# Optimization experiments

Measured on AMD Instinct MI355X. Metric: run time of the kernel, lower is better.

## Reference

```python
import jax, jax.numpy as jnp
import numpy as np

DIM = 768
HEADS = 12
HIDDEN = 3072  # int(dim * mlp_ratio)
DEGREE = 3
EPS = 1e-5


def layer_norm(x, g, b):
    m = jnp.mean(x, axis=-1, keepdims=True)
    v = jnp.mean((x - m) ** 2, axis=-1, keepdims=True)
    return (x - m) * jax.lax.rsqrt(v + EPS) * g + b


def cheby_layer(x, coeffs):
    # x: (B, N, I); coeffs: (I, O, DEGREE+1)
    t = jnp.tanh(x)
    theta = jnp.arccos(t)  # (B, N, I)
    d = jnp.arange(DEGREE + 1, dtype=x.dtype)
    basis = jnp.cos(theta[..., None] * d)  # (B, N, I, D)
    return jnp.einsum('bnid,iod->bno', basis, coeffs)


def setup_inputs() -> dict:
    key = jax.random.key(0)
    ks = jax.random.split(key, 9)
    B, N, C, H = 32, 197, DIM, HIDDEN
    x = jax.random.normal(ks[0], (B, N, C), dtype=jnp.float32)
    g1 = jnp.ones((C,), jnp.float32)
    b1 = jnp.zeros((C,), jnp.float32)
    w_qkv = jax.random.normal(ks[1], (C, 3 * C), jnp.float32) * (C ** -0.5)
    w_proj = jax.random.normal(ks[2], (C, C), jnp.float32) * (C ** -0.5)
    b_proj = jnp.zeros((C,), jnp.float32)
    g2 = jnp.ones((C,), jnp.float32)
    b2 = jnp.zeros((C,), jnp.float32)
    c1 = jax.random.normal(ks[3], (C, H, DEGREE + 1), jnp.float32) / (C * (DEGREE + 1))
    c2 = jax.random.normal(ks[4], (H, C, DEGREE + 1), jnp.float32) / (H * (DEGREE + 1))
    return {"x": x, "g1": g1, "b1": b1, "w_qkv": w_qkv, "w_proj": w_proj,
            "b_proj": b_proj, "g2": g2, "b2": b2, "c1": c1, "c2": c2}


def reference(x, g1, b1, w_qkv, w_proj, b_proj, g2, b2, c1, c2):
    B, N, C = x.shape
    hd = C // HEADS
    scale = hd ** -0.5
    # --- attention branch ---
    h = layer_norm(x, g1, b1)
    qkv = (h @ w_qkv).reshape(B, N, 3, HEADS, hd).transpose(2, 0, 3, 1, 4)
    q, k, v = qkv[0], qkv[1], qkv[2]  # (B, H, N, hd)
    attn = jax.nn.softmax(jnp.einsum('bhnd,bhmd->bhnm', q, k) * scale, axis=-1)
    o = jnp.einsum('bhnm,bhmd->bhnd', attn, v).transpose(0, 2, 1, 3).reshape(B, N, C)
    x = x + o @ w_proj + b_proj
    # --- ChebyKAN MLP branch ---
    h = layer_norm(x, g2, b2)
    h = cheby_layer(h, c1)   # (B, N, HIDDEN)
    h = cheby_layer(h, c2)   # (B, N, C)
    return x + h
```

## Files before the change

kernel.cpp:

```cpp
#include <hip/hip_runtime.h>
#include <hip/hip_bf16.h>
#include <cmath>
#include <cstdint>
#include <cstddef>

#define DEV __device__ __forceinline__

typedef __attribute__((ext_vector_type(4))) float f32x4;
typedef __attribute__((ext_vector_type(8))) short bf16x8;
typedef __attribute__((ext_vector_type(4))) unsigned int u32x4;
typedef __attribute__((ext_vector_type(4))) unsigned short u16x4;

constexpr int NBATCH = 32;
constexpr int SEQ    = 197;
constexpr int CH     = 768;
constexpr int H3     = 3 * CH;
constexpr int NHEADS = 12;
constexpr int HD     = 64;
constexpr int HID    = 3072;
constexpr int TOK    = NBATCH * SEQ;
constexpr int TOKP   = 6400;
constexpr int KSPLIT = 4;
constexpr float LNEPS = 1e-5f;

DEV unsigned short f2bf(float f) {
  unsigned int u = __builtin_bit_cast(unsigned int, f);
  u += 0x7fffu + ((u >> 16) & 1u);
  return (unsigned short)(u >> 16);
}
DEV float bf2f(unsigned short s) {
  unsigned int u = ((unsigned int)s) << 16;
  return __builtin_bit_cast(float, u);
}

DEV void async_copy16(void* lds, const void* gmem) {
  __builtin_amdgcn_global_load_lds(
      (const __attribute__((address_space(1))) unsigned int*)gmem,
      (__attribute__((address_space(3))) unsigned int*)lds, 16, 0, 0);
}

template <int DO_TANH>
__global__ void ln_kernel(const float* __restrict__ xin, const float* __restrict__ gg,
                          const float* __restrict__ bb, unsigned short* __restrict__ outp) {
  const int row  = blockIdx.x * 4 + (threadIdx.x >> 6);
  const int lane = threadIdx.x & 63;
  if (row >= TOK) {
    u16x4 z = {0, 0, 0, 0};
    #pragma unroll
    for (int c = 0; c < 3; ++c)
      *(u16x4*)&outp[(size_t)row * CH + c * 256 + lane * 4] = z;
    return;
  }
  f32x4 v[3];
  float s = 0.f, s2 = 0.f;
  #pragma unroll
  for (int c = 0; c < 3; ++c) {
    v[c] = *(const f32x4*)&xin[(size_t)row * CH + c * 256 + lane * 4];
    #pragma unroll
    for (int e = 0; e < 4; ++e) { s += v[c][e]; s2 += v[c][e] * v[c][e]; }
  }
  #pragma unroll
  for (int off = 32; off; off >>= 1) { s += __shfl_xor(s, off); s2 += __shfl_xor(s2, off); }
  const float mean = s * (1.f / CH);
  const float var  = s2 * (1.f / CH) - mean * mean;
  const float rs   = rsqrtf(var + LNEPS);
  #pragma unroll
  for (int c = 0; c < 3; ++c) {
    f32x4 gv = *(const f32x4*)&gg[c * 256 + lane * 4];
    f32x4 bv = *(const f32x4*)&bb[c * 256 + lane * 4];
    u16x4 o;
    #pragma unroll
    for (int e = 0; e < 4; ++e) {
      float f = (v[c][e] - mean) * rs * gv[e] + bv[e];
      if (DO_TANH) f = tanhf(f);
      o[e] = f2bf(f);
    }
    *(u16x4*)&outp[(size_t)row * CH + c * 256 + lane * 4] = o;
  }
}

__global__ void transpose_bf16(const float* __restrict__ in, unsigned short* __restrict__ outp,
                               int K, int N) {
  __shared__ unsigned short tile[64][65];
  const int k0 = blockIdx.x * 64, n0 = blockIdx.y * 64;
  const int tc = threadIdx.x & 63, tr = threadIdx.x >> 6;
  #pragma unroll
  for (int rr = 0; rr < 64; rr += 4)
    tile[rr + tr][tc] = f2bf(in[(size_t)(k0 + rr + tr) * N + n0 + tc]);
  __syncthreads();
  #pragma unroll
  for (int rr = 0; rr < 64; rr += 4)
    outp[(size_t)(n0 + rr + tr) * K + k0 + tc] = tile[tc][rr + tr];
}

__global__ void cheb_combine(const float* __restrict__ cc, unsigned short* __restrict__ outp,
                             float* __restrict__ partial, int I, int O) {
  __shared__ unsigned short t1[64][65];
  __shared__ unsigned short t2[64][65];
  __shared__ unsigned short t3[64][65];
  __shared__ float psum[4][64];
  const int i0 = blockIdx.x * 64, o0 = blockIdx.y * 64;
  const int tc = threadIdx.x & 63, tr = threadIdx.x >> 6;
  float bs = 0.f;
  #pragma unroll
  for (int rr = 0; rr < 64; rr += 4) {
    f32x4 v = *(const f32x4*)&cc[((size_t)(i0 + rr + tr) * O + (o0 + tc)) * 4];
    t1[rr + tr][tc] = f2bf(v[1] - 3.f * v[3]);
    t2[rr + tr][tc] = f2bf(2.f * v[2]);
    t3[rr + tr][tc] = f2bf(4.f * v[3]);
    bs += v[0] - v[2];
  }
  psum[tr][tc] = bs;
  __syncthreads();
  const size_t K3 = (size_t)3 * I;
  #pragma unroll
  for (int rr = 0; rr < 64; rr += 4) {
    size_t ob = (size_t)(o0 + rr + tr) * K3 + i0 + tc;
    outp[ob]         = t1[tc][rr + tr];
    outp[ob + I]     = t2[tc][rr + tr];
    outp[ob + 2 * I] = t3[tc][rr + tr];
  }
  if (tr == 0)
    partial[(size_t)blockIdx.x * O + o0 + tc] =
        psum[0][tc] + psum[1][tc] + psum[2][tc] + psum[3][tc];
}

__global__ void bias_finish(const float* __restrict__ partial, float* __restrict__ bias,
                            int nblk, int O) {
  const int o = blockIdx.x * 256 + threadIdx.x;
  float s = 0.f;
  for (int k = 0; k < nblk; ++k) s += partial[(size_t)k * O + o];
  bias[o] = s;
}

__global__ void zero_pad_rows(unsigned short* __restrict__ p) {
  const size_t idx = ((size_t)blockIdx.x * 256 + threadIdx.x) * 4;
  u16x4 z = {0, 0, 0, 0};
  *(u16x4*)&p[(size_t)TOK * CH + idx] = z;
}

template <int EPI>
__global__ __launch_bounds__(256)
void gemm_kernel(const unsigned short* __restrict__ A,
                 const unsigned short* __restrict__ BT,
                 const int K, const int Nn,
                 const float* __restrict__ bias,
                 const float* __restrict__ resid,
                 void* __restrict__ Cout) {
  __shared__ __align__(16) unsigned short As[2][128 * 32];
  __shared__ __align__(16) unsigned short Bs[2][128 * 32];
  const int t = threadIdx.x;
  const int lane = t & 63;
  const int wid = t >> 6;
  const int wm = wid >> 1, wn = wid & 1;
  const int bm = blockIdx.x * 128;
  const int bn = blockIdx.y * 128;
  const int srow = t >> 2;
  const int scol = (t & 3) * 8;
  f32x4 acc[4][4] = {};
  const int nkt = K >> 5;

  auto stage = [&](int buf, int kt) {
    const int kk = kt << 5;
    char* lb = (char*)&Bs[buf][0] + (wid << 10);
    async_copy16(lb,        &BT[(size_t)(bn + srow) * K + kk + scol]);
    async_copy16(lb + 4096, &BT[(size_t)(bn + 64 + srow) * K + kk + scol]);
    char* la = (char*)&As[buf][0] + (wid << 10);
    async_copy16(la,        &A[(size_t)(bm + srow) * K + kk + scol]);
    async_copy16(la + 4096, &A[(size_t)(bm + 64 + srow) * K + kk + scol]);
  };

  int cur = 0;
  stage(0, 0);
  for (int kt = 0; kt < nkt; ++kt) {
    if (kt + 1 < nkt) {
      stage(cur ^ 1, kt + 1);
      asm volatile("s_waitcnt vmcnt(4)" ::: "memory");
    } else {
      asm volatile("s_waitcnt vmcnt(0)" ::: "memory");
    }
    __builtin_amdgcn_s_barrier();
    __builtin_amdgcn_sched_barrier(0);
    bf16x8 af[4], bfr[4];
    const int frow = lane & 15;
    const int fk = (lane >> 4) * 8;
    #pragma unroll
    for (int m = 0; m < 4; ++m)
      af[m] = *(const bf16x8*)&As[cur][(wm * 64 + m * 16 + frow) * 32 + fk];
    #pragma unroll
    for (int n = 0; n < 4; ++n)
      bfr[n] = *(const bf16x8*)&Bs[cur][(wn * 64 + n * 16 + frow) * 32 + fk];
    #pragma unroll
    for (int m = 0; m < 4; ++m)
      #pragma unroll
      for (int n = 0; n < 4; ++n)
        acc[m][n] = __builtin_amdgcn_mfma_f32_16x16x32_bf16(af[m], bfr[n], acc[m][n], 0, 0, 0);
    __builtin_amdgcn_s_barrier();
    cur ^= 1;
  }
  #pragma unroll
  for (int m = 0; m < 4; ++m) {
    #pragma unroll
    for (int n = 0; n < 4; ++n) {
      #pragma unroll
      for (int r = 0; r < 4; ++r) {
        const int row = bm + wm * 64 + m * 16 + (lane >> 4) * 4 + r;
        const int col = bn + wn * 64 + n * 16 + (lane & 15);
        const float v = acc[m][n][r];
        if (EPI == 0) {
          ((unsigned short*)Cout)[(size_t)row * Nn + col] = f2bf(v);
        } else {
          float o = 0.f;
          if (row < TOK) o = v + bias[col] + resid[(size_t)row * Nn + col];
          ((float*)Cout)[(size_t)row * Nn + col] = o;
        }
      }
    }
  }
}

template <int EPI>
__global__ __launch_bounds__(256, 2)
void cheb_gemm(const unsigned short* __restrict__ A,
               const unsigned short* __restrict__ BT,
               const int I, const int Nn,
               const float* __restrict__ bias,
               void* __restrict__ Cout) {
  __shared__ __align__(16) unsigned short As[2][128 * 32];
  __shared__ __align__(16) unsigned short Bs[2][3 * 128 * 32];
  const int t = threadIdx.x, lane = t & 63, wid = t >> 6;
  const int wm = wid >> 1, wn = wid & 1;
  const int bm = blockIdx.x * 128, bn = blockIdx.y * 128;
  const int srow = t >> 2, scol = (t & 3) * 8;
  const int K3 = 3 * I;
  const int chunk = I / gridDim.z;
  const int kbase = blockIdx.z * chunk;
  const int nkt = chunk >> 5;
  f32x4 acc[4][4] = {};

  auto stage = [&](int buf, int kt) {
    const int kk = kbase + (kt << 5);
    char* la = (char*)&As[buf][0] + (wid << 10);
    async_copy16(la,        &A[(size_t)(bm + srow) * I + kk + scol]);
    async_copy16(la + 4096, &A[(size_t)(bm + 64 + srow) * I + kk + scol]);
    char* lb = (char*)&Bs[buf][0] + (wid << 10);
    #pragma unroll
    for (int p = 0; p < 3; ++p) {
      async_copy16(lb + p * 8192,        &BT[(size_t)(bn + srow) * K3 + p * I + kk + scol]);
      async_copy16(lb + p * 8192 + 4096, &BT[(size_t)(bn + 64 + srow) * K3 + p * I + kk + scol]);
    }
  };

  int cur = 0;
  stage(0, 0);
  for (int kt = 0; kt < nkt; ++kt) {
    if (kt + 1 < nkt) {
      stage(cur ^ 1, kt + 1);
      asm volatile("s_waitcnt vmcnt(8)" ::: "memory");
    } else {
      asm volatile("s_waitcnt vmcnt(0)" ::: "memory");
    }
    __builtin_amdgcn_s_barrier();
    __builtin_amdgcn_sched_barrier(0);
    const int frow = lane & 15, fk = (lane >> 4) * 8;
    bf16x8 af1[4], af2[4], af3[4];
    #pragma unroll
    for (int m = 0; m < 4; ++m)
      af1[m] = *(const bf16x8*)&As[cur][(wm * 64 + m * 16 + frow) * 32 + fk];
    #pragma unroll
    for (int m = 0; m < 4; ++m) {
      const unsigned int* w = (const unsigned int*)&af1[m];
      unsigned int sq[4], cu[4];
      #pragma unroll
      for (int j = 0; j < 4; ++j) {
        const unsigned int u = w[j];
        const float lo = __builtin_bit_cast(float, u << 16);
        const float hi = __builtin_bit_cast(float, u & 0xffff0000u);
        const float lo2 = lo * lo, hi2 = hi * hi;
        const float lo3 = lo2 * lo, hi3 = hi2 * hi;
        sq[j] = (__builtin_bit_cast(unsigned int, hi2) & 0xffff0000u) |
                (__builtin_bit_cast(unsigned int, lo2) >> 16);
        cu[j] = (__builtin_bit_cast(unsigned int, hi3) & 0xffff0000u) |
                (__builtin_bit_cast(unsigned int, lo3) >> 16);
      }
      af2[m] = *(const bf16x8*)sq;
      af3[m] = *(const bf16x8*)cu;
    }
    #pragma unroll
    for (int p = 0; p < 3; ++p) {
      bf16x8 bfr[4];
      #pragma unroll
      for (int n = 0; n < 4; ++n)
        bfr[n] = *(const bf16x8*)&Bs[cur][(p * 128 + wn * 64 + n * 16 + frow) * 32 + fk];
      #pragma unroll
      for (int m = 0; m < 4; ++m) {
        const bf16x8 a = (p == 0) ? af1[m] : (p == 1) ? af2[m] : af3[m];
        #pragma unroll
        for (int n = 0; n < 4; ++n)
          acc[m][n] = __builtin_amdgcn_mfma_f32_16x16x32_bf16(a, bfr[n], acc[m][n], 0, 0, 0);
      }
    }
    __builtin_amdgcn_s_barrier();
    cur ^= 1;
  }
  #pragma unroll
  for (int m = 0; m < 4; ++m) {
    #pragma unroll
    for (int n = 0; n < 4; ++n) {
      #pragma unroll
      for (int r = 0; r < 4; ++r) {
        const int row = bm + wm * 64 + m * 16 + (lane >> 4) * 4 + r;
        const int col = bn + wn * 64 + n * 16 + (lane & 15);
        const float v = acc[m][n][r];
        if (EPI == 2) {
          ((unsigned short*)Cout)[(size_t)row * Nn + col] = f2bf(tanhf(v + bias[col]));
        } else {
          ((float*)Cout)[((size_t)blockIdx.z * TOKP + row) * Nn + col] = v;
        }
      }
    }
  }
}

__global__ void cheb2_reduce(const float* __restrict__ part, const float* __restrict__ bias,
                             const float* __restrict__ resid, float* __restrict__ outp) {
  const size_t idx = ((size_t)blockIdx.x * 256 + threadIdx.x) * 4;
  const int col = (int)(idx % CH);
  f32x4 s = *(const f32x4*)&part[idx];
  #pragma unroll
  for (int z = 1; z < KSPLIT; ++z) {
    f32x4 p = *(const f32x4*)&part[(size_t)z * TOKP * CH + idx];
    #pragma unroll
    for (int e = 0; e < 4; ++e) s[e] += p[e];
  }
  const f32x4 bv = *(const f32x4*)&bias[col];
  const f32x4 rv = *(const f32x4*)&resid[idx];
  f32x4 o;
  #pragma unroll
  for (int e = 0; e < 4; ++e) o[e] = s[e] + bv[e] + rv[e];
  *(f32x4*)&outp[idx] = o;
}

__global__ __launch_bounds__(256)
void attn_kernel(const unsigned short* __restrict__ qkv, unsigned short* __restrict__ aout) {
  constexpr int VSTR = 232;
  __shared__ __align__(16) unsigned short Vlds[64 * VSTR];
  __shared__ __align__(16) unsigned short Plds[4][16 * VSTR];
  const int bh = blockIdx.x;
  const int b = bh / NHEADS, hh = bh - b * NHEADS;
  const int t = threadIdx.x, lane = t & 63, wid = t >> 6;
  const size_t base = (size_t)b * SEQ * H3;
  const int part = t & 7, key0 = t >> 3;
  for (int it = 0; it < 7; ++it) {
    const int key = key0 + it * 32;
    u32x4 raw = {0, 0, 0, 0};
    if (key < SEQ)
      raw = *(const u32x4*)&qkv[base + (size_t)key * H3 + 2 * CH + hh * HD + part * 8];
    const unsigned short* us = (const unsigned short*)&raw;
    #pragma unroll
    for (int e = 0; e < 8; ++e)
      Vlds[(part * 8 + e) * VSTR + key] = us[e];
  }
  for (int idx = t; idx < 4 * 16 * 16; idx += 256) {
    const int buf = idx >> 8, rr = (idx >> 4) & 15, ccc = idx & 15;
    Plds[buf][rr * VSTR + 208 + ccc] = 0;
  }
  __syncthreads();

  for (int qt = wid; qt < 13; qt += 4) {
    const int qrow = qt * 16 + (lane & 15);
    const size_t qbase = base + (size_t)qrow * H3 + hh * HD + (lane >> 4) * 8;
    const bf16x8 qf0 = *(const bf16x8*)&qkv[qbase];
    const bf16x8 qf1 = *(const bf16x8*)&qkv[qbase + 32];
    float sv[13][4];
    #pragma unroll
    for (int ktile = 0; ktile < 13; ++ktile) {
      const int keyc = ktile * 16 + (lane & 15);
      const size_t kbase = base + (size_t)keyc * H3 + CH + hh * HD + (lane >> 4) * 8;
      const bf16x8 kf0 = *(const bf16x8*)&qkv[kbase];
      const bf16x8 kf1 = *(const bf16x8*)&qkv[kbase + 32];
      f32x4 s = {0.f, 0.f, 0.f, 0.f};
      s = __builtin_amdgcn_mfma_f32_16x16x32_bf16(qf0, kf0, s, 0, 0, 0);
      s = __builtin_amdgcn_mfma_f32_16x16x32_bf16(qf1, kf1, s, 0, 0, 0);
      const bool valid = keyc < SEQ;
      #pragma unroll
      for (int r = 0; r < 4; ++r)
        sv[ktile][r] = valid ? s[r] * 0.125f : -INFINITY;
    }
    float rsum[4];
    #pragma unroll
    for (int r = 0; r < 4; ++r) {
      float mx = -INFINITY;
      #pragma unroll
      for (int kt2 = 0; kt2 < 13; ++kt2) mx = fmaxf(mx, sv[kt2][r]);
      #pragma unroll
      for (int off = 1; off < 16; off <<= 1) mx = fmaxf(mx, __shfl_xor(mx, off));
      float sum = 0.f;
      #pragma unroll
      for (int kt2 = 0; kt2 < 13; ++kt2) {
        const float p = __expf(sv[kt2][r] - mx);
        sv[kt2][r] = p;
        sum += p;
      }
      #pragma unroll
      for (int off = 1; off < 16; off <<= 1) sum += __shfl_xor(sum, off);
      rsum[r] = sum;
    }
    const int g4 = (lane >> 4) * 4;
    #pragma unroll
    for (int kt2 = 0; kt2 < 13; ++kt2)
      #pragma unroll
      for (int r = 0; r < 4; ++r)
        Plds[wid][(g4 + r) * VSTR + kt2 * 16 + (lane & 15)] = f2bf(sv[kt2][r]);
    asm volatile("s_waitcnt lgkmcnt(0)" ::: "memory");
    f32x4 oacc[4] = {};
    #pragma unroll
    for (int ks = 0; ks < 7; ++ks) {
      const bf16x8 pf = *(const bf16x8*)&Plds[wid][(lane & 15) * VSTR + ks * 32 + (lane >> 4) * 8];
      #pragma unroll
      for (int n = 0; n < 4; ++n) {
        const bf16x8 vf = *(const bf16x8*)&Vlds[(n * 16 + (lane & 15)) * VSTR + ks * 32 + (lane >> 4) * 8];
        oacc[n] = __builtin_amdgcn_mfma_f32_16x16x32_bf16(pf, vf, oacc[n], 0, 0, 0);
      }
    }
    #pragma unroll
    for (int n = 0; n < 4; ++n)
      #pragma unroll
      for (int r = 0; r < 4; ++r) {
        const int q = qt * 16 + g4 + r;
        if (q < SEQ) {
          const float val = oacc[n][r] / rsum[r];
          aout[(size_t)(b * SEQ + q) * CH + hh * HD + n * 16 + (lane & 15)] = f2bf(val);
        }
      }
  }
}

extern "C" void kernel_launch(void* const* d_in, const int* in_sizes, int n_in,
                              void* d_out, int out_size, void* d_ws, size_t ws_size,
                              hipStream_t stream) {
  const float* x      = (const float*)d_in[0];
  const float* g1     = (const float*)d_in[1];
  const float* b1     = (const float*)d_in[2];
  const float* w_qkv  = (const float*)d_in[3];
  const float* w_proj = (const float*)d_in[4];
  const float* b_proj = (const float*)d_in[5];
  const float* g2     = (const float*)d_in[6];
  const float* b2     = (const float*)d_in[7];
  const float* c1     = (const float*)d_in[8];
  const float* c2     = (const float*)d_in[9];

  char* ws = (char*)d_ws;
  size_t off = 0;
  auto alloc = [&](size_t bytes) { size_t o = off; off += (bytes + 255) & ~(size_t)255; return o; };
  unsigned short* h      = (unsigned short*)(ws + alloc((size_t)TOKP * CH * 2));
  unsigned short* wqkvT  = (unsigned short*)(ws + alloc((size_t)H3 * CH * 2));
  unsigned short* wprojT = (unsigned short*)(ws + alloc((size_t)CH * CH * 2));
  unsigned short* c1T    = (unsigned short*)(ws + alloc((size_t)HID * 3 * CH * 2));
  unsigned short* c2T    = (unsigned short*)(ws + alloc((size_t)CH * 3 * HID * 2));
  float* bias1           = (float*)(ws + alloc((size_t)HID * 4));
  float* bias2           = (float*)(ws + alloc((size_t)CH * 4));
  float* part1           = (float*)(ws + alloc((size_t)(CH / 64) * HID * 4));
  float* part2           = (float*)(ws + alloc((size_t)(HID / 64) * CH * 4));
  unsigned short* qkvb   = (unsigned short*)(ws + alloc((size_t)TOKP * H3 * 2));
  unsigned short* aoutb  = (unsigned short*)(ws + alloc((size_t)TOKP * CH * 2));
  float* xmid            = (float*)(ws + alloc((size_t)TOKP * CH * 4));
  unsigned short* t1b    = (unsigned short*)(ws + alloc((size_t)TOKP * CH * 2));
  unsigned short* t2b    = (unsigned short*)(ws + alloc((size_t)TOKP * HID * 2));
  float* partK           = (float*)(ws + alloc((size_t)KSPLIT * TOKP * CH * 4));
  (void)ws_size; (void)in_sizes; (void)n_in; (void)out_size;

  transpose_bf16<<<dim3(CH / 64, H3 / 64), 256, 0, stream>>>(w_qkv, wqkvT, CH, H3);
  transpose_bf16<<<dim3(CH / 64, CH / 64), 256, 0, stream>>>(w_proj, wprojT, CH, CH);
  cheb_combine<<<dim3(CH / 64, HID / 64), 256, 0, stream>>>(c1, c1T, part1, CH, HID);
  cheb_combine<<<dim3(HID / 64, CH / 64), 256, 0, stream>>>(c2, c2T, part2, HID, CH);
  bias_finish<<<dim3(HID / 256), 256, 0, stream>>>(part1, bias1, CH / 64, HID);
  bias_finish<<<dim3(CH / 256), 256, 0, stream>>>(part2, bias2, HID / 64, CH);
  zero_pad_rows<<<dim3(72), 256, 0, stream>>>(aoutb);

  ln_kernel<0><<<dim3(TOKP / 4), 256, 0, stream>>>(x, g1, b1, h);
  gemm_kernel<0><<<dim3(TOKP / 128, H3 / 128), 256, 0, stream>>>(h, wqkvT, CH, H3,
                                                                 nullptr, nullptr, qkvb);
  attn_kernel<<<dim3(NBATCH * NHEADS), 256, 0, stream>>>(qkvb, aoutb);
  gemm_kernel<1><<<dim3(TOKP / 128, CH / 128), 256, 0, stream>>>(aoutb, wprojT, CH, CH,
                                                                 b_proj, x, xmid);
  ln_kernel<1><<<dim3(TOKP / 4), 256, 0, stream>>>(xmid, g2, b2, t1b);
  cheb_gemm<2><<<dim3(TOKP / 128, HID / 128, 1), 256, 0, stream>>>(t1b, c1T, CH, HID,
                                                                   bias1, t2b);
  cheb_gemm<4><<<dim3(TOKP / 128, CH / 128, KSPLIT), 256, 0, stream>>>(t2b, c2T, HID, CH,
                                                                       nullptr, partK);
  cheb2_reduce<<<dim3(TOK * CH / 1024), 256, 0, stream>>>(partK, bias2, xmid, (float*)d_out);
}
```

Baseline: 429.6 us.

## Retile Chebyshev GEMMs to 128x64, drop split-K reduction, use fast tanh

Changes the Chebyshev GEMM tile from 128x128 to 128x64 with each wave owning 32 rows, and raises launch bounds so more blocks fit per CU. The combined coefficients move to a plane-major layout so each of the three basis planes is read as its own contiguous block. The second Chebyshev GEMM no longer splits K four ways into a partial buffer followed by a reduce kernel. It now applies bias and residual directly in its epilogue, which removes the large partial buffer traffic and one launch at the cost of longer per-block K loops. tanhf is replaced by an exp and reciprocal approximation, which trades a little accuracy for cheaper arithmetic.

```diff
diff --git a/kernel.cpp b/kernel.cpp
--- a/kernel.cpp
+++ b/kernel.cpp
@@ -20,7 +20,6 @@
 constexpr int HID    = 3072;
 constexpr int TOK    = NBATCH * SEQ;
 constexpr int TOKP   = 6400;
-constexpr int KSPLIT = 4;
 constexpr float LNEPS = 1e-5f;
 
 DEV unsigned short f2bf(float f) {
@@ -31,6 +30,11 @@
 DEV float bf2f(unsigned short s) {
   unsigned int u = ((unsigned int)s) << 16;
   return __builtin_bit_cast(float, u);
+}
+
+DEV float fast_tanh(float x) {
+  const float e = __expf(2.f * x);
+  return 1.f - 2.f * __builtin_amdgcn_rcpf(e + 1.f);
 }
 
 DEV void async_copy16(void* lds, const void* gmem) {
@@ -72,7 +76,7 @@
     #pragma unroll
     for (int e = 0; e < 4; ++e) {
       float f = (v[c][e] - mean) * rs * gv[e] + bv[e];
-      if (DO_TANH) f = tanhf(f);
+      if (DO_TANH) f = fast_tanh(f);
       o[e] = f2bf(f);
     }
     *(u16x4*)&outp[(size_t)row * CH + c * 256 + lane * 4] = o;
@@ -112,13 +116,13 @@
   }
   psum[tr][tc] = bs;
   __syncthreads();
-  const size_t K3 = (size_t)3 * I;
+  const size_t plane = (size_t)O * I;
   #pragma unroll
   for (int rr = 0; rr < 64; rr += 4) {
-    size_t ob = (size_t)(o0 + rr + tr) * K3 + i0 + tc;
-    outp[ob]         = t1[tc][rr + tr];
-    outp[ob + I]     = t2[tc][rr + tr];
-    outp[ob + 2 * I] = t3[tc][rr + tr];
+    size_t ob = (size_t)(o0 + rr + tr) * I + i0 + tc;
+    outp[ob]             = t1[tc][rr + tr];
+    outp[ob + plane]     = t2[tc][rr + tr];
+    outp[ob + 2 * plane] = t3[tc][rr + tr];
   }
   if (tr == 0)
     partial[(size_t)blockIdx.x * O + o0 + tc] =
@@ -143,7 +147,7 @@
 __global__ __launch_bounds__(256)
 void gemm_kernel(const unsigned short* __restrict__ A,
                  const unsigned short* __restrict__ BT,
-                 const int K, const int Nn,
+                 const int Ktot, const int Nn,
                  const float* __restrict__ bias,
                  const float* __restrict__ resid,
                  void* __restrict__ Cout) {
@@ -157,17 +161,17 @@
   const int bn = blockIdx.y * 128;
   const int srow = t >> 2;
   const int scol = (t & 3) * 8;
+  const int nkt = Ktot >> 5;
   f32x4 acc[4][4] = {};
-  const int nkt = K >> 5;
 
   auto stage = [&](int buf, int kt) {
     const int kk = kt << 5;
     char* lb = (char*)&Bs[buf][0] + (wid << 10);
-    async_copy16(lb,        &BT[(size_t)(bn + srow) * K + kk + scol]);
-    async_copy16(lb + 4096, &BT[(size_t)(bn + 64 + srow) * K + kk + scol]);
+    async_copy16(lb,        &BT[(size_t)(bn + srow) * Ktot + kk + scol]);
+    async_copy16(lb + 4096, &BT[(size_t)(bn + 64 + srow) * Ktot + kk + scol]);
     char* la = (char*)&As[buf][0] + (wid << 10);
-    async_copy16(la,        &A[(size_t)(bm + srow) * K + kk + scol]);
-    async_copy16(la + 4096, &A[(size_t)(bm + 64 + srow) * K + kk + scol]);
+    async_copy16(la,        &A[(size_t)(bm + srow) * Ktot + kk + scol]);
+    async_copy16(la + 4096, &A[(size_t)(bm + 64 + srow) * Ktot + kk + scol]);
   };
 
   int cur = 0;
@@ -220,35 +224,30 @@
 }
 
 template <int EPI>
-__global__ __launch_bounds__(256, 2)
+__global__ __launch_bounds__(256, 4)
 void cheb_gemm(const unsigned short* __restrict__ A,
                const unsigned short* __restrict__ BT,
-               const int I, const int Nn,
+               const int Ktot, const int Nn,
                const float* __restrict__ bias,
+               const float* __restrict__ resid,
                void* __restrict__ Cout) {
   __shared__ __align__(16) unsigned short As[2][128 * 32];
-  __shared__ __align__(16) unsigned short Bs[2][3 * 128 * 32];
+  __shared__ __align__(16) unsigned short Bs[2][3 * 64 * 32];
   const int t = threadIdx.x, lane = t & 63, wid = t >> 6;
-  const int wm = wid >> 1, wn = wid & 1;
-  const int bm = blockIdx.x * 128, bn = blockIdx.y * 128;
+  const int bm = blockIdx.x * 128, bn = blockIdx.y * 64;
   const int srow = t >> 2, scol = (t & 3) * 8;
-  const int K3 = 3 * I;
-  const int chunk = I / gridDim.z;
-  const int kbase = blockIdx.z * chunk;
-  const int nkt = chunk >> 5;
-  f32x4 acc[4][4] = {};
+  const int nkt = Ktot >> 5;
+  f32x4 acc[2][4] = {};
 
   auto stage = [&](int buf, int kt) {
-    const int kk = kbase + (kt << 5);
+    const int kk = kt << 5;
     char* la = (char*)&As[buf][0] + (wid << 10);
-    async_copy16(la,        &A[(size_t)(bm + srow) * I + kk + scol]);
-    async_copy16(la + 4096, &A[(size_t)(bm + 64 + srow) * I + kk + scol]);
+    async_copy16(la,        &A[(size_t)(bm + srow) * Ktot + kk + scol]);
+    async_copy16(la + 4096, &A[(size_t)(bm + 64 + srow) * Ktot + kk + scol]);
     char* lb = (char*)&Bs[buf][0] + (wid << 10);
     #pragma unroll
-    for (int p = 0; p < 3; ++p) {
-      async_copy16(lb + p * 8192,        &BT[(size_t)(bn + srow) * K3 + p * I + kk + scol]);
-      async_copy16(lb + p * 8192 + 4096, &BT[(size_t)(bn + 64 + srow) * K3 + p * I + kk + scol]);
-    }
+    for (int p = 0; p < 3; ++p)
+      async_copy16(lb + p * 4096, &BT[((size_t)p * Nn + bn + srow) * Ktot + kk + scol]);
   };
 
   int cur = 0;
@@ -256,20 +255,20 @@
   for (int kt = 0; kt < nkt; ++kt) {
     if (kt + 1 < nkt) {
       stage(cur ^ 1, kt + 1);
-      asm volatile("s_waitcnt vmcnt(8)" ::: "memory");
+      asm volatile("s_waitcnt vmcnt(5)" ::: "memory");
     } else {
       asm volatile("s_waitcnt vmcnt(0)" ::: "memory");
     }
     __builtin_amdgcn_s_barrier();
     __builtin_amdgcn_sched_barrier(0);
     const int frow = lane & 15, fk = (lane >> 4) * 8;
-    bf16x8 af1[4], af2[4], af3[4];
-    #pragma unroll
-    for (int m = 0; m < 4; ++m)
-      af1[m] = *(const bf16x8*)&As[cur][(wm * 64 + m * 16 + frow) * 32 + fk];
-    #pragma unroll
-    for (int m = 0; m < 4; ++m) {
-      const unsigned int* w = (const unsigned int*)&af1[m];
+    bf16x8 a1[2], a2[2], a3[2];
+    #pragma unroll
+    for (int m = 0; m < 2; ++m)
+      a1[m] = *(const bf16x8*)&As[cur][(wid * 32 + m * 16 + frow) * 32 + fk];
+    #pragma unroll
+    for (int m = 0; m < 2; ++m) {
+      const unsigned int* w = (const unsigned int*)&a1[m];
       unsigned int sq[4], cu[4];
       #pragma unroll
       for (int j = 0; j < 4; ++j) {
@@ -283,62 +282,44 @@
         cu[j] = (__builtin_bit_cast(unsigned int, hi3) & 0xffff0000u) |
                 (__builtin_bit_cast(unsigned int, lo3) >> 16);
       }
-      af2[m] = *(const bf16x8*)sq;
-      af3[m] = *(const bf16x8*)cu;
+      a2[m] = *(const bf16x8*)sq;
+      a3[m] = *(const bf16x8*)cu;
     }
     #pragma unroll
     for (int p = 0; p < 3; ++p) {
-      bf16x8 bfr[4];
+      bf16x8 br[4];
       #pragma unroll
       for (int n = 0; n < 4; ++n)
-        bfr[n] = *(const bf16x8*)&Bs[cur][(p * 128 + wn * 64 + n * 16 + frow) * 32 + fk];
-      #pragma unroll
-      for (int m = 0; m < 4; ++m) {
-        const bf16x8 a = (p == 0) ? af1[m] : (p == 1) ? af2[m] : af3[m];
+        br[n] = *(const bf16x8*)&Bs[cur][(p * 64 + n * 16 + frow) * 32 + fk];
+      #pragma unroll
+      for (int m = 0; m < 2; ++m) {
+        const bf16x8 a = (p == 0) ? a1[m] : (p == 1) ? a2[m] : a3[m];
         #pragma unroll
         for (int n = 0; n < 4; ++n)
-          acc[m][n] = __builtin_amdgcn_mfma_f32_16x16x32_bf16(a, bfr[n], acc[m][n], 0, 0, 0);
+          acc[m][n] = __builtin_amdgcn_mfma_f32_16x16x32_bf16(a, br[n], acc[m][n], 0, 0, 0);
       }
     }
     __builtin_amdgcn_s_barrier();
     cur ^= 1;
   }
   #pragma unroll
-  for (int m = 0; m < 4; ++m) {
+  for (int m = 0; m < 2; ++m) {
     #pragma unroll
     for (int n = 0; n < 4; ++n) {
       #pragma unroll
       for (int r = 0; r < 4; ++r) {
-        const int row = bm + wm * 64 + m * 16 + (lane >> 4) * 4 + r;
-        const int col = bn + wn * 64 + n * 16 + (lane & 15);
+        const int row = bm + wid * 32 + m * 16 + (lane >> 4) * 4 + r;
+        const int col = bn + n * 16 + (lane & 15);
         const float v = acc[m][n][r];
-        if (EPI == 2) {
-          ((unsigned short*)Cout)[(size_t)row * Nn + col] = f2bf(tanhf(v + bias[col]));
+        if (EPI == 0) {
+          ((unsigned short*)Cout)[(size_t)row * Nn + col] = f2bf(fast_tanh(v + bias[col]));
         } else {
-          ((float*)Cout)[((size_t)blockIdx.z * TOKP + row) * Nn + col] = v;
+          if (row < TOK)
+            ((float*)Cout)[(size_t)row * Nn + col] = v + bias[col] + resid[(size_t)row * Nn + col];
         }
       }
     }
   }
-}
-
-__global__ void cheb2_reduce(const float* __restrict__ part, const float* __restrict__ bias,
-                             const float* __restrict__ resid, float* __restrict__ outp) {
-  const size_t idx = ((size_t)blockIdx.x * 256 + threadIdx.x) * 4;
-  const int col = (int)(idx % CH);
-  f32x4 s = *(const f32x4*)&part[idx];
-  #pragma unroll
-  for (int z = 1; z < KSPLIT; ++z) {
-    f32x4 p = *(const f32x4*)&part[(size_t)z * TOKP * CH + idx];
-    #pragma unroll
-    for (int e = 0; e < 4; ++e) s[e] += p[e];
-  }
-  const f32x4 bv = *(const f32x4*)&bias[col];
-  const f32x4 rv = *(const f32x4*)&resid[idx];
-  f32x4 o;
-  #pragma unroll
-  for (int e = 0; e < 4; ++e) o[e] = s[e] + bv[e] + rv[e];
-  *(f32x4*)&outp[idx] = o;
 }
 
 __global__ __launch_bounds__(256)
@@ -456,8 +437,8 @@
   unsigned short* h      = (unsigned short*)(ws + alloc((size_t)TOKP * CH * 2));
   unsigned short* wqkvT  = (unsigned short*)(ws + alloc((size_t)H3 * CH * 2));
   unsigned short* wprojT = (unsigned short*)(ws + alloc((size_t)CH * CH * 2));
-  unsigned short* c1T    = (unsigned short*)(ws + alloc((size_t)HID * 3 * CH * 2));
-  unsigned short* c2T    = (unsigned short*)(ws + alloc((size_t)CH * 3 * HID * 2));
+  unsigned short* c1T    = (unsigned short*)(ws + alloc((size_t)3 * HID * CH * 2));
+  unsigned short* c2T    = (unsigned short*)(ws + alloc((size_t)3 * CH * HID * 2));
   float* bias1           = (float*)(ws + alloc((size_t)HID * 4));
   float* bias2           = (float*)(ws + alloc((size_t)CH * 4));
   float* part1           = (float*)(ws + alloc((size_t)(CH / 64) * HID * 4));
@@ -465,9 +446,8 @@
   unsigned short* qkvb   = (unsigned short*)(ws + alloc((size_t)TOKP * H3 * 2));
   unsigned short* aoutb  = (unsigned short*)(ws + alloc((size_t)TOKP * CH * 2));
   float* xmid            = (float*)(ws + alloc((size_t)TOKP * CH * 4));
-  unsigned short* t1b    = (unsigned short*)(ws + alloc((size_t)TOKP * CH * 2));
-  unsigned short* t2b    = (unsigned short*)(ws + alloc((size_t)TOKP * HID * 2));
-  float* partK           = (float*)(ws + alloc((size_t)KSPLIT * TOKP * CH * 4));
+  unsigned short* tb     = (unsigned short*)(ws + alloc((size_t)TOKP * CH * 2));
+  unsigned short* ub     = (unsigned short*)(ws + alloc((size_t)TOKP * HID * 2));
   (void)ws_size; (void)in_sizes; (void)n_in; (void)out_size;
 
   transpose_bf16<<<dim3(CH / 64, H3 / 64), 256, 0, stream>>>(w_qkv, wqkvT, CH, H3);
@@ -484,10 +464,9 @@
   attn_kernel<<<dim3(NBATCH * NHEADS), 256, 0, stream>>>(qkvb, aoutb);
   gemm_kernel<1><<<dim3(TOKP / 128, CH / 128), 256, 0, stream>>>(aoutb, wprojT, CH, CH,
                                                                  b_proj, x, xmid);
-  ln_kernel<1><<<dim3(TOKP / 4), 256, 0, stream>>>(xmid, g2, b2, t1b);
-  cheb_gemm<2><<<dim3(TOKP / 128, HID / 128, 1), 256, 0, stream>>>(t1b, c1T, CH, HID,
-                                                                   bias1, t2b);
-  cheb_gemm<4><<<dim3(TOKP / 128, CH / 128, KSPLIT), 256, 0, stream>>>(t2b, c2T, HID, CH,
-                                                                       nullptr, partK);
-  cheb2_reduce<<<dim3(TOK * CH / 1024), 256, 0, stream>>>(partK, bias2, xmid, (float*)d_out);
-}
+  ln_kernel<1><<<dim3(TOKP / 4), 256, 0, stream>>>(xmid, g2, b2, tb);
+  cheb_gemm<0><<<dim3(TOKP / 128, HID / 64), 256, 0, stream>>>(tb, c1T, CH, HID,
+                                                               bias1, nullptr, ub);
+  cheb_gemm<1><<<dim3(TOKP / 128, CH / 64), 256, 0, stream>>>(ub, c2T, HID, CH,
+                                                              bias2, xmid, (float*)d_out);
+}
```

Measured after the change: 412.0 us. -4.1%, faster.
